# Optimization experiments

Measured on AMD Instinct MI355X. Metric: run time of the kernel, lower is better.

Reference implementation:

```python
import jax, jax.numpy as jnp
import numpy as np

EMBED_DIM = 1024
NUM_HEADS = 16
HEAD_DIM = EMBED_DIM // NUM_HEADS
WINDOW = 128


def setup_inputs() -> dict:
    key = jax.random.key(0)
    ks = jax.random.split(key, 11)
    B, S, E = 2, 2048, EMBED_DIM
    scale = 1.0 / np.sqrt(E)
    inp = {
        "q": jax.random.normal(ks[0], (B, S, E), jnp.float32),
        "k": jax.random.normal(ks[1], (B, S, E), jnp.float32),
        "v": jax.random.normal(ks[2], (B, S, E), jnp.float32),
        "Wq": jax.random.normal(ks[3], (E, E), jnp.float32) * scale,
        "bq": jnp.zeros((E,), jnp.float32),
        "Wk": jax.random.normal(ks[4], (E, E), jnp.float32) * scale,
        "bk": jnp.zeros((E,), jnp.float32),
        "Wv": jax.random.normal(ks[5], (E, E), jnp.float32) * scale,
        "bv": jnp.zeros((E,), jnp.float32),
        "Wo": jax.random.normal(ks[6], (E, E), jnp.float32) * scale,
        "bo": jnp.zeros((E,), jnp.float32),
    }
    return inp


def reference(q, k, v, Wq, bq, Wk, bk, Wv, bv, Wo, bo):
    B, S, E = q.shape
    H, D = NUM_HEADS, HEAD_DIM
    # projections (torch Linear: x @ W.T + b)
    Q = (q @ Wq.T + bq).reshape(B, S, H, D).transpose(0, 2, 1, 3)  # [B,H,S,D]
    K = (k @ Wk.T + bk).reshape(B, S, H, D).transpose(0, 2, 1, 3)
    V = (v @ Wv.T + bv).reshape(B, S, H, D).transpose(0, 2, 1, 3)
    scores = jnp.einsum("bhqd,bhkd->bhqk", Q, K) / jnp.sqrt(jnp.float32(D))
    idx = jnp.arange(S)
    band = jnp.abs(idx[:, None] - idx[None, :]) <= WINDOW  # [S,S] bool band mask
    scores = jnp.where(band[None, None], scores, -jnp.inf)
    probs = jax.nn.softmax(scores, axis=-1)
    out = jnp.einsum("bhqk,bhkd->bhqd", probs, V)  # [B,H,S,D]
    out = out.transpose(0, 2, 1, 3).reshape(B, S, E)
    return out @ Wo.T + bo
```

## Files before the change

### kernel.cpp

```cpp
#include <hip/hip_runtime.h>


#define S_LEN 2048
#define EMB   1024
#define NHEAD 16
#define HDIM  64
#define MROWS 4096

typedef __attribute__((ext_vector_type(4))) float f32x4;
typedef __attribute__((ext_vector_type(8))) short bf16x8;

__device__ __forceinline__ unsigned short f2bf(float x){
  union { float f; unsigned u; } un; un.f = x;
  unsigned u = un.u;
  unsigned r = (u + 0x7FFFu + ((u >> 16) & 1u)) >> 16;
  return (unsigned short)r;
}

__global__ __launch_bounds__(256) void cvt3_kernel(
    const float4* __restrict__ s0, const float4* __restrict__ s1,
    const float4* __restrict__ s2,
    unsigned long long* __restrict__ d0, unsigned long long* __restrict__ d1,
    unsigned long long* __restrict__ d2)
{
  int i = blockIdx.x * 256 + threadIdx.x;
  const float4* s = (blockIdx.y == 0) ? s0 : (blockIdx.y == 1) ? s1 : s2;
  unsigned long long* d = (blockIdx.y == 0) ? d0 : (blockIdx.y == 1) ? d1 : d2;
  float4 v = s[i];
  d[i] = (unsigned long long)f2bf(v.x)
       | ((unsigned long long)f2bf(v.y) << 16)
       | ((unsigned long long)f2bf(v.z) << 32)
       | ((unsigned long long)f2bf(v.w) << 48);
}

__global__ __launch_bounds__(256) void cvt4_kernel(
    const float4* __restrict__ s0, const float4* __restrict__ s1,
    const float4* __restrict__ s2, const float4* __restrict__ s3,
    unsigned long long* __restrict__ d0, unsigned long long* __restrict__ d1,
    unsigned long long* __restrict__ d2, unsigned long long* __restrict__ d3)
{
  int i = blockIdx.x * 256 + threadIdx.x;
  const float4* s = (blockIdx.y == 0) ? s0 : (blockIdx.y == 1) ? s1 :
                    (blockIdx.y == 2) ? s2 : s3;
  unsigned long long* d = (blockIdx.y == 0) ? d0 : (blockIdx.y == 1) ? d1 :
                          (blockIdx.y == 2) ? d2 : d3;
  float4 v = s[i];
  d[i] = (unsigned long long)f2bf(v.x)
       | ((unsigned long long)f2bf(v.y) << 16)
       | ((unsigned long long)f2bf(v.z) << 32)
       | ((unsigned long long)f2bf(v.w) << 48);
}

__device__ __forceinline__ void async_copy16(const unsigned short* g, unsigned short* l){
  __builtin_amdgcn_global_load_lds(
      (const __attribute__((address_space(1))) unsigned int*)(const void*)g,
      (__attribute__((address_space(3))) unsigned int*)(void*)l,
      16, 0, 0);
}

__device__ __forceinline__ void gemm_core_128(
    const unsigned short* __restrict__ A,
    const unsigned short* __restrict__ Bw,
    unsigned short* lds,
    int tile_m, int tile_n, f32x4 acc[4][4])
{
  const int tid  = threadIdx.x;
  const int lane = tid & 63;
  const int wid  = tid >> 6;
  const int wm = wid >> 1, wn = wid & 1;
  const int c = lane & 15, g = lane >> 4;
  const int srow = lane >> 3, sch = lane & 7;

  unsigned short* As0 = lds;
  unsigned short* Bs0 = lds + 8192;
  unsigned short* As1 = lds + 16384;
  unsigned short* Bs1 = lds + 24576;

  auto stage = [&](unsigned short* As, unsigned short* Bs, int k0){
#pragma unroll
    for (int i = 0; i < 4; ++i){
      int row = (wid*4 + i)*8 + srow;
      int chg = sch ^ (row & 7);
      async_copy16(A  + (size_t)(tile_m + row)*EMB + k0 + chg*8, As + (wid*4 + i)*512);
      async_copy16(Bw + (size_t)(tile_n + row)*EMB + k0 + chg*8, Bs + (wid*4 + i)*512);
    }
  };

  auto compute = [&](const unsigned short* As, const unsigned short* Bs){
#pragma unroll
    for (int kk = 0; kk < 2; ++kk){
      bf16x8 af[4], bfv[4];
#pragma unroll
      for (int mi = 0; mi < 4; ++mi){
        int row = wm*64 + mi*16 + c;
        int ch  = (kk*4 + g) ^ (row & 7);
        af[mi] = *(const bf16x8*)&As[row*64 + ch*8];
      }
#pragma unroll
      for (int ni = 0; ni < 4; ++ni){
        int row = wn*64 + ni*16 + c;
        int ch  = (kk*4 + g) ^ (row & 7);
        bfv[ni] = *(const bf16x8*)&Bs[row*64 + ch*8];
      }
#pragma unroll
      for (int mi = 0; mi < 4; ++mi)
#pragma unroll
        for (int ni = 0; ni < 4; ++ni)
          acc[mi][ni] = __builtin_amdgcn_mfma_f32_16x16x32_bf16(af[mi], bfv[ni], acc[mi][ni], 0, 0, 0);
    }
  };

  stage(As0, Bs0, 0);
  __syncthreads();
  for (int t = 0; t < 16; t += 2){
    stage(As1, Bs1, (t+1)*64);
    compute(As0, Bs0);
    __syncthreads();
    if (t + 2 < 16) stage(As0, Bs0, (t+2)*64);
    compute(As1, Bs1);
    __syncthreads();
  }
}

__global__ __launch_bounds__(256) void qkv_gemm_kernel(
    const unsigned short* __restrict__ qb, const unsigned short* __restrict__ kb2,
    const unsigned short* __restrict__ vb,
    const unsigned short* __restrict__ Wqb, const unsigned short* __restrict__ Wkb,
    const unsigned short* __restrict__ Wvb,
    const float* __restrict__ bq, const float* __restrict__ bk,
    const float* __restrict__ bv,
    unsigned short* __restrict__ Qp, unsigned short* __restrict__ Kp,
    unsigned short* __restrict__ Vt)
{
  __shared__ __align__(16) unsigned short lds[4*8192];
  const int z = blockIdx.z;
  const unsigned short* A    = (z == 0) ? qb  : (z == 1) ? kb2 : vb;
  const unsigned short* W    = (z == 0) ? Wqb : (z == 1) ? Wkb : Wvb;
  const float*          bias = (z == 0) ? bq  : (z == 1) ? bk  : bv;
  const int tile_m = blockIdx.x * 128;
  const int tile_n = blockIdx.y * 128;
  f32x4 acc[4][4] = {};
  gemm_core_128(A, W, lds, tile_m, tile_n, acc);

  const int tid = threadIdx.x, lane = tid & 63, wid = tid >> 6;
  const int wm = wid >> 1, wn = wid & 1, c = lane & 15, g = lane >> 4;

  if (z < 2){
    unsigned short* O = (z == 0) ? Qp : Kp;
#pragma unroll
    for (int mi = 0; mi < 4; ++mi){
      int m0 = tile_m + wm*64 + mi*16 + g*4;
#pragma unroll
      for (int ni = 0; ni < 4; ++ni){
        int n = tile_n + wn*64 + ni*16 + c;
        int h = n >> 6, d = n & 63;
        float bvn = bias[n];
#pragma unroll
        for (int j = 0; j < 4; ++j){
          int m = m0 + j;
          int bb = m >> 11, ss = m & 2047;
          O[(((size_t)bb*NHEAD + h)*S_LEN + ss)*HDIM + d] = f2bf(acc[mi][ni][j] + bvn);
        }
      }
    }
  } else {
#pragma unroll
    for (int mi = 0; mi < 4; ++mi){
      int m0 = tile_m + wm*64 + mi*16 + g*4;
      int bb = m0 >> 11, ss = m0 & 2047;
      int ssp = (ss & ~31) | (((ss >> 2) & 3) << 3) | (((ss >> 4) & 1) << 2);
#pragma unroll
      for (int ni = 0; ni < 4; ++ni){
        int n = tile_n + wn*64 + ni*16 + c;
        int h = n >> 6, d = n & 63;
        float bvn = bias[n];
        unsigned long long pk =
              (unsigned long long)f2bf(acc[mi][ni][0] + bvn)
            | ((unsigned long long)f2bf(acc[mi][ni][1] + bvn) << 16)
            | ((unsigned long long)f2bf(acc[mi][ni][2] + bvn) << 32)
            | ((unsigned long long)f2bf(acc[mi][ni][3] + bvn) << 48);
        *(unsigned long long*)&Vt[(((size_t)bb*NHEAD + h)*HDIM + d)*S_LEN + ssp] = pk;
      }
    }
  }
}

__global__ __launch_bounds__(256) void attn_kernel(
    const unsigned short* __restrict__ Qp, const unsigned short* __restrict__ Kp,
    const unsigned short* __restrict__ Vt, unsigned short* __restrict__ X2)
{
  __shared__ __align__(16) unsigned short Kl[2][64*64];
  __shared__ __align__(16) unsigned short Vl[2][64*64];

  const int tid = threadIdx.x, lane = tid & 63, w = tid >> 6;
  const int c = lane & 15, g = lane >> 4;
  int bid0 = blockIdx.x;
  int bid = (bid0 & 7) * 128 + (bid0 >> 3);
  const int bh = bid >> 5, qt = bid & 31;
  const int qbase = qt * 64;
  const int qw = qbase + w * 16;
  const int qi = qw + c;

  const unsigned short* Kbh = Kp + (size_t)bh * S_LEN * HDIM;
  const unsigned short* Vbh = Vt + (size_t)bh * HDIM * S_LEN;

  const unsigned short* Qb = Qp + ((size_t)bh*S_LEN + qw + c)*HDIM;
  bf16x8 aq0 = *(const bf16x8*)(Qb + g*8);
  bf16x8 aq1 = *(const bf16x8*)(Qb + 32 + g*8);

  f32x4 accO[4] = {};
  float lsum = 0.f;
  const float SC = 0.18033688011112042f;

  int t0 = qbase - 128; if (t0 < 0) t0 = 0;
  int t1 = qbase + 192; if (t1 > S_LEN) t1 = S_LEN;

  const int srow = lane >> 3;
  const int sch  = (lane & 7) ^ srow;

  auto stage = [&](int buf, int kt){
#pragma unroll
    for (int i = 0; i < 2; ++i){
      int r0 = w*16 + i*8;
      async_copy16(Kbh + (size_t)(kt + r0 + srow)*HDIM + sch*8,
                   &Kl[buf][r0*64]);
      async_copy16(Vbh + (size_t)(r0 + srow)*S_LEN + kt + sch*8,
                   &Vl[buf][r0*64]);
    }
  };

  auto compute = [&](int buf, int kt){
    f32x4 s[4];
    __builtin_amdgcn_s_setprio(1);
#pragma unroll
    for (int f = 0; f < 4; ++f){
      const unsigned short* Kr = &Kl[buf][(f*16 + c)*64];
      bf16x8 k0 = *(const bf16x8*)(Kr + ((    g) ^ (c & 7))*8);
      bf16x8 k1 = *(const bf16x8*)(Kr + ((4 + g) ^ (c & 7))*8);
      f32x4 a = {0.f, 0.f, 0.f, 0.f};
      a = __builtin_amdgcn_mfma_f32_16x16x32_bf16(k0, aq0, a, 0, 0, 0);
      a = __builtin_amdgcn_mfma_f32_16x16x32_bf16(k1, aq1, a, 0, 0, 0);
      s[f] = a;
    }
    __builtin_amdgcn_s_setprio(0);

    float p[4][4];
    bool nomask = (kt >= qw - 113) && (kt <= qw + 65);
    if (nomask){
#pragma unroll
      for (int f = 0; f < 4; ++f)
#pragma unroll
        for (int j = 0; j < 4; ++j){
          p[f][j] = exp2f(s[f][j] * SC);
          lsum += p[f][j];
        }
    } else {
#pragma unroll
      for (int f = 0; f < 4; ++f)
#pragma unroll
        for (int j = 0; j < 4; ++j){
          int dlt = qi - (kt + f*16 + g*4 + j);
          float e = exp2f(s[f][j] * SC);
          e = (dlt <= 128 && dlt >= -128) ? e : 0.f;
          p[f][j] = e;
          lsum += e;
        }
    }

    union { unsigned u[4]; bf16x8 v; } A0, A1;
    A0.u[0] = (unsigned)f2bf(p[0][0]) | ((unsigned)f2bf(p[0][1]) << 16);
    A0.u[1] = (unsigned)f2bf(p[0][2]) | ((unsigned)f2bf(p[0][3]) << 16);
    A0.u[2] = (unsigned)f2bf(p[1][0]) | ((unsigned)f2bf(p[1][1]) << 16);
    A0.u[3] = (unsigned)f2bf(p[1][2]) | ((unsigned)f2bf(p[1][3]) << 16);
    A1.u[0] = (unsigned)f2bf(p[2][0]) | ((unsigned)f2bf(p[2][1]) << 16);
    A1.u[1] = (unsigned)f2bf(p[2][2]) | ((unsigned)f2bf(p[2][3]) << 16);
    A1.u[2] = (unsigned)f2bf(p[3][0]) | ((unsigned)f2bf(p[3][1]) << 16);
    A1.u[3] = (unsigned)f2bf(p[3][2]) | ((unsigned)f2bf(p[3][3]) << 16);

    __builtin_amdgcn_s_setprio(1);
#pragma unroll
    for (int dblk = 0; dblk < 4; ++dblk){
      const unsigned short* Vr = &Vl[buf][(dblk*16 + c)*64];
      bf16x8 v0 = *(const bf16x8*)(Vr + ((    g) ^ (c & 7))*8);
      bf16x8 v1 = *(const bf16x8*)(Vr + ((4 + g) ^ (c & 7))*8);
      accO[dblk] = __builtin_amdgcn_mfma_f32_16x16x32_bf16(A0.v, v0, accO[dblk], 0, 0, 0);
      accO[dblk] = __builtin_amdgcn_mfma_f32_16x16x32_bf16(A1.v, v1, accO[dblk], 0, 0, 0);
    }
    __builtin_amdgcn_s_setprio(0);
  };

  stage(0, t0);
  __syncthreads();
  int cur = 0;
  for (int kt = t0; kt < t1; kt += 64){
    if (kt + 64 < t1) stage(cur ^ 1, kt + 64);
    bool active = (kt + 63 >= qw - 128) && (kt <= qw + 143);
    if (active) compute(cur, kt);
    __syncthreads();
    cur ^= 1;
  }

  lsum += __shfl_xor(lsum, 16);
  lsum += __shfl_xor(lsum, 32);
  float rl[4];
#pragma unroll
  for (int j = 0; j < 4; ++j)
    rl[j] = 1.f / __shfl(lsum, g*4 + j);

  const int b_ = bh >> 4, h_ = bh & 15;
#pragma unroll
  for (int dblk = 0; dblk < 4; ++dblk)
#pragma unroll
    for (int j = 0; j < 4; ++j){
      int s_ = qw + g*4 + j, d_ = dblk*16 + c;
      X2[((size_t)(b_*S_LEN + s_))*EMB + h_*64 + d_] = f2bf(accO[dblk][j] * rl[j]);
    }
}

__global__ __launch_bounds__(256) void out_gemm_kernel(
    const unsigned short* __restrict__ X2, const unsigned short* __restrict__ Wob,
    const float* __restrict__ bo, float* __restrict__ out)
{
  __shared__ __align__(16) unsigned short lds[4*8192];
  const int tile_m = blockIdx.x * 128;
  const int tile_n = blockIdx.y * 128;
  f32x4 acc[4][4] = {};
  gemm_core_128(X2, Wob, lds, tile_m, tile_n, acc);

  const int tid = threadIdx.x, lane = tid & 63, wid = tid >> 6;
  const int wm = wid >> 1, wn = wid & 1, c = lane & 15, g = lane >> 4;
#pragma unroll
  for (int mi = 0; mi < 4; ++mi){
    int m0 = tile_m + wm*64 + mi*16 + g*4;
#pragma unroll
    for (int ni = 0; ni < 4; ++ni){
      int n = tile_n + wn*64 + ni*16 + c;
      float bvn = bo[n];
#pragma unroll
      for (int j = 0; j < 4; ++j)
        out[(size_t)(m0 + j)*EMB + n] = acc[mi][ni][j] + bvn;
    }
  }
}

extern "C" void kernel_launch(void* const* d_in, const int* in_sizes, int n_in,
                              void* d_out, int out_size, void* d_ws, size_t ws_size,
                              hipStream_t stream)
{
  const float* q  = (const float*)d_in[0];
  const float* k  = (const float*)d_in[1];
  const float* v  = (const float*)d_in[2];
  const float* Wq = (const float*)d_in[3];
  const float* bq = (const float*)d_in[4];
  const float* Wk = (const float*)d_in[5];
  const float* bk = (const float*)d_in[6];
  const float* Wv = (const float*)d_in[7];
  const float* bv = (const float*)d_in[8];
  const float* Wo = (const float*)d_in[9];
  const float* bo = (const float*)d_in[10];
  float* out = (float*)d_out;

  unsigned short* ws = (unsigned short*)d_ws;
  unsigned short* qb  = ws;
  unsigned short* kb  = ws + 4194304;
  unsigned short* vb  = ws + 8388608;
  unsigned short* Wqb = ws + 12582912;
  unsigned short* Wkb = ws + 13631488;
  unsigned short* Wvb = ws + 14680064;
  unsigned short* Wob = ws + 15728640;
  unsigned short* Qp  = ws + 16777216;
  unsigned short* Kp  = ws + 20971520;
  unsigned short* Vt  = ws + 25165824;
  unsigned short* X2  = qb;

  cvt3_kernel<<<dim3(4096, 3), 256, 0, stream>>>(
      (const float4*)q, (const float4*)k, (const float4*)v,
      (unsigned long long*)qb, (unsigned long long*)kb, (unsigned long long*)vb);
  cvt4_kernel<<<dim3(1024, 4), 256, 0, stream>>>(
      (const float4*)Wq, (const float4*)Wk, (const float4*)Wv, (const float4*)Wo,
      (unsigned long long*)Wqb, (unsigned long long*)Wkb,
      (unsigned long long*)Wvb, (unsigned long long*)Wob);

  qkv_gemm_kernel<<<dim3(32, 8, 3), 256, 0, stream>>>(
      qb, kb, vb, Wqb, Wkb, Wvb, bq, bk, bv, Qp, Kp, Vt);

  attn_kernel<<<1024, 256, 0, stream>>>(Qp, Kp, Vt, X2);

  out_gemm_kernel<<<dim3(32, 8), 256, 0, stream>>>(X2, Wob, bo, out);
}
```

Measured before the change: 88.97 us.

## Rewrite QKV GEMM with 256x256 tiles, 512 threads, and interleaved async prefetch

Replaces the 128x128 QKV projection GEMM (768 blocks of 256 threads) with a 256x256-tile kernel of 512 threads over 192 blocks, using a flat grid with an XCD-aware block swizzle. K-tiles are double-buffered in LDS with async copies spread across the four compute sub-phases, controlled by explicit vmcnt waits and barriers. The aim is more operand reuse per LDS load and better overlap of global loads with MFMA. The cost is 128 KB of LDS per block and more accumulator registers. With only 192 blocks, there may be too few to fill all CUs.

```diff
diff --git a/kernel.cpp b/kernel.cpp
--- a/kernel.cpp
+++ b/kernel.cpp
@@ -122,7 +122,7 @@
   }
 }
 
-__global__ __launch_bounds__(256) void qkv_gemm_kernel(
+__global__ __launch_bounds__(512, 2) void qkv_gemm_kernel(
     const unsigned short* __restrict__ qb, const unsigned short* __restrict__ kb2,
     const unsigned short* __restrict__ vb,
     const unsigned short* __restrict__ Wqb, const unsigned short* __restrict__ Wkb,
@@ -132,53 +132,121 @@
     unsigned short* __restrict__ Qp, unsigned short* __restrict__ Kp,
     unsigned short* __restrict__ Vt)
 {
-  __shared__ __align__(16) unsigned short lds[4*8192];
-  const int z = blockIdx.z;
-  const unsigned short* A    = (z == 0) ? qb  : (z == 1) ? kb2 : vb;
-  const unsigned short* W    = (z == 0) ? Wqb : (z == 1) ? Wkb : Wvb;
-  const float*          bias = (z == 0) ? bq  : (z == 1) ? bk  : bv;
-  const int tile_m = blockIdx.x * 128;
-  const int tile_n = blockIdx.y * 128;
-  f32x4 acc[4][4] = {};
-  gemm_core_128(A, W, lds, tile_m, tile_n, acc);
+  __shared__ __align__(16) unsigned short lds[2][2][256*64];
 
   const int tid = threadIdx.x, lane = tid & 63, wid = tid >> 6;
-  const int wm = wid >> 1, wn = wid & 1, c = lane & 15, g = lane >> 4;
+  const int wm = wid >> 2, wn = wid & 3;
+  const int c = lane & 15, g = lane >> 4;
+  const int srow = lane >> 3, sch = lane & 7;
+
+  int bid  = blockIdx.x;
+  int bid2 = (bid & 7) * 24 + (bid >> 3);
+  const int mx = bid2 & 15, ny = bid2 >> 4;
+  const int z  = ny >> 2;
+  const int tile_m = mx * 256;
+  const int nloc   = (ny & 3) * 256;
+
+  const unsigned short* A = (z == 0) ? qb  : (z == 1) ? kb2 : vb;
+  const unsigned short* W = (z == 0) ? Wqb : (z == 1) ? Wkb : Wvb;
+  const float*       bias = (z == 0) ? bq  : (z == 1) ? bk  : bv;
+
+  const unsigned short* Asrc = A + (size_t)tile_m * EMB;
+  const unsigned short* Bsrc = W + (size_t)nloc * EMB;
+
+  f32x4 acc[8][4] = {};
+
+  auto stageP = [&](int b, int k0, int p){
+    int row = wid*32 + p*8 + srow;
+    int ch  = sch ^ (row & 7);
+    async_copy16(Asrc + (size_t)row*EMB + k0 + ch*8, &lds[b][0][(wid*32 + p*8)*64]);
+    async_copy16(Bsrc + (size_t)row*EMB + k0 + ch*8, &lds[b][1][(wid*32 + p*8)*64]);
+  };
+
+  stageP(0, 0, 0); stageP(0, 0, 1); stageP(0, 0, 2); stageP(0, 0, 3);
+
+  for (int t = 0; t < 16; ++t){
+    const int cb = t & 1, nb = cb ^ 1;
+    const bool pre = (t < 15);
+    const int k1 = (t + 1) * 64;
+
+    if (pre){
+      stageP(nb, k1, 0);
+      asm volatile("s_waitcnt vmcnt(2)" ::: "memory");
+    } else {
+      asm volatile("s_waitcnt vmcnt(0)" ::: "memory");
+    }
+    asm volatile("s_barrier" ::: "memory");
+
+    bf16x8 bfr[4][2];
+#pragma unroll
+    for (int ni = 0; ni < 4; ++ni)
+#pragma unroll
+      for (int kk = 0; kk < 2; ++kk){
+        int row = wn*64 + ni*16 + c;
+        int ch  = (kk*4 + g) ^ (row & 7);
+        bfr[ni][kk] = *(const bf16x8*)&lds[cb][1][row*64 + ch*8];
+      }
+
+#pragma unroll
+    for (int p = 0; p < 4; ++p){
+      bf16x8 af[2][2];
+#pragma unroll
+      for (int mi = 0; mi < 2; ++mi)
+#pragma unroll
+        for (int kk = 0; kk < 2; ++kk){
+          int row = wm*128 + (p*2 + mi)*16 + c;
+          int ch  = (kk*4 + g) ^ (row & 7);
+          af[mi][kk] = *(const bf16x8*)&lds[cb][0][row*64 + ch*8];
+        }
+      if (pre && p > 0) stageP(nb, k1, p);
+      asm volatile("s_barrier" ::: "memory");
+      __builtin_amdgcn_s_setprio(1);
+#pragma unroll
+      for (int kk = 0; kk < 2; ++kk)
+#pragma unroll
+        for (int mi = 0; mi < 2; ++mi)
+#pragma unroll
+          for (int ni = 0; ni < 4; ++ni)
+            acc[p*2 + mi][ni] = __builtin_amdgcn_mfma_f32_16x16x32_bf16(
+                af[mi][kk], bfr[ni][kk], acc[p*2 + mi][ni], 0, 0, 0);
+      __builtin_amdgcn_s_setprio(0);
+      asm volatile("s_barrier" ::: "memory");
+    }
+  }
 
   if (z < 2){
     unsigned short* O = (z == 0) ? Qp : Kp;
 #pragma unroll
-    for (int mi = 0; mi < 4; ++mi){
-      int m0 = tile_m + wm*64 + mi*16 + g*4;
+    for (int mf = 0; mf < 8; ++mf){
+      int m0 = tile_m + wm*128 + mf*16 + g*4;
+      int bb = m0 >> 11, ss = m0 & 2047;
 #pragma unroll
       for (int ni = 0; ni < 4; ++ni){
-        int n = tile_n + wn*64 + ni*16 + c;
-        int h = n >> 6, d = n & 63;
-        float bvn = bias[n];
-#pragma unroll
-        for (int j = 0; j < 4; ++j){
-          int m = m0 + j;
-          int bb = m >> 11, ss = m & 2047;
-          O[(((size_t)bb*NHEAD + h)*S_LEN + ss)*HDIM + d] = f2bf(acc[mi][ni][j] + bvn);
-        }
+        int nn = nloc + wn*64 + ni*16 + c;
+        int h = nn >> 6, d = nn & 63;
+        float bvn = bias[nn];
+        size_t base = (((size_t)bb*NHEAD + h)*S_LEN + ss)*HDIM + d;
+#pragma unroll
+        for (int j = 0; j < 4; ++j)
+          O[base + (size_t)j*HDIM] = f2bf(acc[mf][ni][j] + bvn);
       }
     }
   } else {
 #pragma unroll
-    for (int mi = 0; mi < 4; ++mi){
-      int m0 = tile_m + wm*64 + mi*16 + g*4;
+    for (int mf = 0; mf < 8; ++mf){
+      int m0 = tile_m + wm*128 + mf*16 + g*4;
       int bb = m0 >> 11, ss = m0 & 2047;
       int ssp = (ss & ~31) | (((ss >> 2) & 3) << 3) | (((ss >> 4) & 1) << 2);
 #pragma unroll
       for (int ni = 0; ni < 4; ++ni){
-        int n = tile_n + wn*64 + ni*16 + c;
-        int h = n >> 6, d = n & 63;
-        float bvn = bias[n];
+        int nn = nloc + wn*64 + ni*16 + c;
+        int h = nn >> 6, d = nn & 63;
+        float bvn = bias[nn];
         unsigned long long pk =
-              (unsigned long long)f2bf(acc[mi][ni][0] + bvn)
-            | ((unsigned long long)f2bf(acc[mi][ni][1] + bvn) << 16)
-            | ((unsigned long long)f2bf(acc[mi][ni][2] + bvn) << 32)
-            | ((unsigned long long)f2bf(acc[mi][ni][3] + bvn) << 48);
+              (unsigned long long)f2bf(acc[mf][ni][0] + bvn)
+            | ((unsigned long long)f2bf(acc[mf][ni][1] + bvn) << 16)
+            | ((unsigned long long)f2bf(acc[mf][ni][2] + bvn) << 32)
+            | ((unsigned long long)f2bf(acc[mf][ni][3] + bvn) << 48);
         *(unsigned long long*)&Vt[(((size_t)bb*NHEAD + h)*HDIM + d)*S_LEN + ssp] = pk;
       }
     }
@@ -222,10 +290,8 @@
 #pragma unroll
     for (int i = 0; i < 2; ++i){
       int r0 = w*16 + i*8;
-      async_copy16(Kbh + (size_t)(kt + r0 + srow)*HDIM + sch*8,
-                   &Kl[buf][r0*64]);
-      async_copy16(Vbh + (size_t)(r0 + srow)*S_LEN + kt + sch*8,
-                   &Vl[buf][r0*64]);
+      async_copy16(Kbh + (size_t)(kt + r0 + srow)*HDIM + sch*8, &Kl[buf][r0*64]);
+      async_copy16(Vbh + (size_t)(r0 + srow)*S_LEN + kt + sch*8, &Vl[buf][r0*64]);
     }
   };
 
@@ -381,7 +447,7 @@
       (unsigned long long*)Wqb, (unsigned long long*)Wkb,
       (unsigned long long*)Wvb, (unsigned long long*)Wob);
 
-  qkv_gemm_kernel<<<dim3(32, 8, 3), 256, 0, stream>>>(
+  qkv_gemm_kernel<<<dim3(192), 512, 0, stream>>>(
       qb, kb, vb, Wqb, Wkb, Wvb, bq, bk, bv, Qp, Kp, Vt);
 
   attn_kernel<<<1024, 256, 0, stream>>>(Qp, Kp, Vt, X2);
```

Result: no change. 89.79 us (+0.9%).

## Merge conversion kernels and use partial vmcnt waits for double-buffered staging

Applied to the files above, without the earlier changes.

The seven fp32-to-bf16 conversions now run in one launch, with early exit for the smaller weight slices, removing one kernel launch. In the GEMM core and attention loops, the full __syncthreads after prefetch is replaced by a partial s_waitcnt vmcnt plus raw s_barrier. This lets the next tile's async global-to-LDS loads stay in flight while the current tile is computed. The hand-counted vmcnt values must match the number of outstanding loads issued per stage, or reads could race with incomplete copies. The merged conversion grid also launches many idle blocks for the weight slices.

```diff
diff --git a/kernel.cpp b/kernel.cpp
--- a/kernel.cpp
+++ b/kernel.cpp
@@ -17,38 +17,36 @@
   return (unsigned short)r;
 }
 
-__global__ __launch_bounds__(256) void cvt3_kernel(
-    const float4* __restrict__ s0, const float4* __restrict__ s1,
-    const float4* __restrict__ s2,
-    unsigned long long* __restrict__ d0, unsigned long long* __restrict__ d1,
-    unsigned long long* __restrict__ d2)
+__global__ __launch_bounds__(256) void cvt7_kernel(
+    const float4* __restrict__ q,  const float4* __restrict__ k,
+    const float4* __restrict__ v,
+    const float4* __restrict__ Wq, const float4* __restrict__ Wk,
+    const float4* __restrict__ Wv, const float4* __restrict__ Wo,
+    unsigned long long* __restrict__ dq, unsigned long long* __restrict__ dk,
+    unsigned long long* __restrict__ dv,
+    unsigned long long* __restrict__ dWq, unsigned long long* __restrict__ dWk,
+    unsigned long long* __restrict__ dWv, unsigned long long* __restrict__ dWo)
 {
   int i = blockIdx.x * 256 + threadIdx.x;
-  const float4* s = (blockIdx.y == 0) ? s0 : (blockIdx.y == 1) ? s1 : s2;
-  unsigned long long* d = (blockIdx.y == 0) ? d0 : (blockIdx.y == 1) ? d1 : d2;
-  float4 v = s[i];
-  d[i] = (unsigned long long)f2bf(v.x)
-       | ((unsigned long long)f2bf(v.y) << 16)
-       | ((unsigned long long)f2bf(v.z) << 32)
-       | ((unsigned long long)f2bf(v.w) << 48);
-}
-
-__global__ __launch_bounds__(256) void cvt4_kernel(
-    const float4* __restrict__ s0, const float4* __restrict__ s1,
-    const float4* __restrict__ s2, const float4* __restrict__ s3,
-    unsigned long long* __restrict__ d0, unsigned long long* __restrict__ d1,
-    unsigned long long* __restrict__ d2, unsigned long long* __restrict__ d3)
-{
-  int i = blockIdx.x * 256 + threadIdx.x;
-  const float4* s = (blockIdx.y == 0) ? s0 : (blockIdx.y == 1) ? s1 :
-                    (blockIdx.y == 2) ? s2 : s3;
-  unsigned long long* d = (blockIdx.y == 0) ? d0 : (blockIdx.y == 1) ? d1 :
-                          (blockIdx.y == 2) ? d2 : d3;
-  float4 v = s[i];
-  d[i] = (unsigned long long)f2bf(v.x)
-       | ((unsigned long long)f2bf(v.y) << 16)
-       | ((unsigned long long)f2bf(v.z) << 32)
-       | ((unsigned long long)f2bf(v.w) << 48);
+  int y = blockIdx.y;
+  const float4* s;
+  unsigned long long* d;
+  int n4;
+  switch (y){
+    case 0: s = q;  d = dq;  n4 = 1048576; break;
+    case 1: s = k;  d = dk;  n4 = 1048576; break;
+    case 2: s = v;  d = dv;  n4 = 1048576; break;
+    case 3: s = Wq; d = dWq; n4 = 262144;  break;
+    case 4: s = Wk; d = dWk; n4 = 262144;  break;
+    case 5: s = Wv; d = dWv; n4 = 262144;  break;
+    default:s = Wo; d = dWo; n4 = 262144;  break;
+  }
+  if (i >= n4) return;
+  float4 x = s[i];
+  d[i] = (unsigned long long)f2bf(x.x)
+       | ((unsigned long long)f2bf(x.y) << 16)
+       | ((unsigned long long)f2bf(x.z) << 32)
+       | ((unsigned long long)f2bf(x.w) << 48);
 }
 
 __device__ __forceinline__ void async_copy16(const unsigned short* g, unsigned short* l){
@@ -111,14 +109,20 @@
   };
 
   stage(As0, Bs0, 0);
-  __syncthreads();
-  for (int t = 0; t < 16; t += 2){
-    stage(As1, Bs1, (t+1)*64);
-    compute(As0, Bs0);
-    __syncthreads();
-    if (t + 2 < 16) stage(As0, Bs0, (t+2)*64);
-    compute(As1, Bs1);
-    __syncthreads();
+  for (int t = 0; t < 16; ++t){
+    const unsigned short* Ac = (t & 1) ? As1 : As0;
+    const unsigned short* Bc = (t & 1) ? Bs1 : Bs0;
+    unsigned short*       An = (t & 1) ? As0 : As1;
+    unsigned short*       Bn = (t & 1) ? Bs0 : Bs1;
+    if (t < 15){
+      stage(An, Bn, (t + 1) * 64);
+      asm volatile("s_waitcnt vmcnt(8)" ::: "memory");
+    } else {
+      asm volatile("s_waitcnt vmcnt(0)" ::: "memory");
+    }
+    asm volatile("s_barrier" ::: "memory");
+    compute(Ac, Bc);
+    asm volatile("s_barrier" ::: "memory");
   }
 }
 
@@ -222,10 +226,8 @@
 #pragma unroll
     for (int i = 0; i < 2; ++i){
       int r0 = w*16 + i*8;
-      async_copy16(Kbh + (size_t)(kt + r0 + srow)*HDIM + sch*8,
-                   &Kl[buf][r0*64]);
-      async_copy16(Vbh + (size_t)(r0 + srow)*S_LEN + kt + sch*8,
-                   &Vl[buf][r0*64]);
+      async_copy16(Kbh + (size_t)(kt + r0 + srow)*HDIM + sch*8, &Kl[buf][r0*64]);
+      async_copy16(Vbh + (size_t)(r0 + srow)*S_LEN + kt + sch*8, &Vl[buf][r0*64]);
     }
   };
 
@@ -290,13 +292,18 @@
   };
 
   stage(0, t0);
-  __syncthreads();
   int cur = 0;
   for (int kt = t0; kt < t1; kt += 64){
-    if (kt + 64 < t1) stage(cur ^ 1, kt + 64);
+    if (kt + 64 < t1){
+      stage(cur ^ 1, kt + 64);
+      asm volatile("s_waitcnt vmcnt(4)" ::: "memory");
+    } else {
+      asm volatile("s_waitcnt vmcnt(0)" ::: "memory");
+    }
+    asm volatile("s_barrier" ::: "memory");
     bool active = (kt + 63 >= qw - 128) && (kt <= qw + 143);
     if (active) compute(cur, kt);
-    __syncthreads();
+    asm volatile("s_barrier" ::: "memory");
     cur ^= 1;
   }
 
@@ -373,11 +380,10 @@
   unsigned short* Vt  = ws + 25165824;
   unsigned short* X2  = qb;
 
-  cvt3_kernel<<<dim3(4096, 3), 256, 0, stream>>>(
+  cvt7_kernel<<<dim3(4096, 7), 256, 0, stream>>>(
       (const float4*)q, (const float4*)k, (const float4*)v,
-      (unsigned long long*)qb, (unsigned long long*)kb, (unsigned long long*)vb);
-  cvt4_kernel<<<dim3(1024, 4), 256, 0, stream>>>(
       (const float4*)Wq, (const float4*)Wk, (const float4*)Wv, (const float4*)Wo,
+      (unsigned long long*)qb, (unsigned long long*)kb, (unsigned long long*)vb,
       (unsigned long long*)Wqb, (unsigned long long*)Wkb,
       (unsigned long long*)Wvb, (unsigned long long*)Wob);
 
```

New measurement: 88.72 us. About the same (-0.3%).
